# Kernel optimization log

Hardware: AMD Instinct MI355X
Metric: run time of the kernel (lower is better)

The kernel has to match this reference:

```python
import jax, jax.numpy as jnp
import numpy as np

B, M, F, U = 2048, 64, 512, 512  # batch, number_masks, num_features, units=ceil(F**1.0)

def setup_inputs() -> dict:
    key = jax.random.key(0)
    kx, kw = jax.random.split(key)
    x = jax.random.normal(kx, (B, M, F), dtype=jnp.float32)
    # glorot-uniform style init like keras Dense default
    limit = np.sqrt(6.0 / (F + U)).astype(np.float32)
    W = jax.random.uniform(kw, (M, F, U), dtype=jnp.float32, minval=-limit, maxval=limit)
    b = jnp.zeros((M, U), dtype=jnp.float32)
    return {"x": x, "W": W, "b": b}

def reference(x, W, b):
    # Per-mask Dense applied in a Python loop in the original == one batched GEMM.
    # y[b,m,u] = relu(sum_f x[b,m,f] * W[m,f,u] + b[m,u])
    y = jax.nn.relu(jnp.einsum('bmf,mfu->bmu', x, W) + b[None, :, :])
    # Concatenate along feature axis -> [B, M*U]
    return y.reshape(y.shape[0], -1)
```

## Files before the change

### kernel.cpp

```cpp
#include <hip/hip_runtime.h>
#include <hip/hip_bf16.h>


typedef __attribute__((ext_vector_type(8))) short bf16x8;
typedef __attribute__((ext_vector_type(4))) float f32x4;

#define LDS_S 40

__device__ __forceinline__ unsigned pk_bf16(float a, float b) {
    float2 t; t.x = a; t.y = b;
    __hip_bfloat162 h = __float22bfloat162_rn(t);
    union { __hip_bfloat162 h; unsigned u; } cv;
    cv.h = h;
    return cv.u;
}

__device__ __forceinline__ void gld16(const void* g, void* l) {
    __builtin_amdgcn_global_load_lds(
        (const __attribute__((address_space(1))) void*)g,
        (__attribute__((address_space(3))) void*)l, 16, 0, 0);
}

__global__ void wt_prep_kernel(const float* __restrict__ W, short* __restrict__ Wt) {
    __shared__ short t[64][80];
    const int m   = blockIdx.z;
    const int f0  = blockIdx.y * 64;
    const int u0  = blockIdx.x * 64;
    const int tid = threadIdx.x;
    const int fl  = tid >> 4;
    const int us  = tid & 15;
    #pragma unroll
    for (int i = 0; i < 4; ++i) {
        const int f = fl + 16 * i;
        float4 v = *(const float4*)(W + ((size_t)m * 512 + f0 + f) * 512 + u0 + us * 4);
        t[us * 4 + 0][f] = (short)(pk_bf16(v.x, v.x) & 0xffff);
        t[us * 4 + 1][f] = (short)(pk_bf16(v.y, v.y) & 0xffff);
        t[us * 4 + 2][f] = (short)(pk_bf16(v.z, v.z) & 0xffff);
        t[us * 4 + 3][f] = (short)(pk_bf16(v.w, v.w) & 0xffff);
    }
    __syncthreads();
    const int ur = tid >> 3;
    const int fs = tid & 7;
    #pragma unroll
    for (int i = 0; i < 2; ++i) {
        const int u = ur + 32 * i;
        *(uint4*)(Wt + ((size_t)m * 512 + u0 + u) * 512 + f0 + fs * 8) =
            *(const uint4*)&t[u][fs * 8];
    }
}

__global__ __launch_bounds__(256, 3) void pdense_main(const float* __restrict__ X,
                                                      const short* __restrict__ Wt,
                                                      const float* __restrict__ bias,
                                                      float* __restrict__ Out) {
    __shared__ float ldsA[2][128 * 32];
    __shared__ short ldsB[2][128 * 32];

    const int tid  = threadIdx.x;
    const int lane = tid & 63;
    const int wave = tid >> 6;
    const int q    = lane >> 4;
    const int ln   = lane & 15;
    const int wr   = (wave >> 1) * 64;
    const int wc   = (wave & 1) * 64;

    const int id   = blockIdx.x;
    const int xcd  = id & 7;
    const int slot = id >> 3;
    const int m    = xcd * 8 + (slot >> 6);
    const int rem  = slot & 63;
    const int bt   = rem >> 2;
    const int ut   = rem & 3;
    const int row0 = bt * 128;
    const int col0 = ut * 128;

    const int arow = wave * 32 + (lane >> 3);
    const int ac   = (lane & 7) ^ (lane >> 3);
    const float* agp = X + (size_t)(row0 + arow) * 32768 + m * 512 + ac * 4;
    const int brow = wave * 32 + (lane >> 2);
    const int bc   = (lane & 3) ^ ((lane >> 3) & 3);
    const short* bgp = Wt + (size_t)m * 262144 + (size_t)(col0 + brow) * 512 + bc * 8;

    f32x4 acc[4][4];
    #pragma unroll
    for (int i = 0; i < 4; ++i)
        #pragma unroll
        for (int j = 0; j < 4; ++j)
            acc[i][j] = (f32x4)0.0f;

    #pragma unroll
    for (int i = 0; i < 4; ++i)
        gld16(agp + (size_t)i * 8 * 32768, &ldsA[0][(wave * 32 + i * 8) * 32]);
    #pragma unroll
    for (int j = 0; j < 2; ++j)
        gld16(bgp + (size_t)j * 16 * 512, &ldsB[0][(wave * 32 + j * 16) * 32]);

    const int s1 = (ln >> 1) & 3;
    const int s0 = ln & 1;

    for (int kt = 0; kt < 16; ++kt) {
        const int p = kt & 1;

        __builtin_amdgcn_sched_barrier(0);
        __builtin_amdgcn_s_barrier();
        __builtin_amdgcn_sched_barrier(0);

        if (kt + 1 < 16) {
            const int ko = (kt + 1) * 32;
            #pragma unroll
            for (int i = 0; i < 4; ++i)
                gld16(agp + ko + (size_t)i * 8 * 32768, &ldsA[p ^ 1][(wave * 32 + i * 8) * 32]);
            #pragma unroll
            for (int j = 0; j < 2; ++j)
                gld16(bgp + ko + (size_t)j * 16 * 512, &ldsB[p ^ 1][(wave * 32 + j * 16) * 32]);
            __builtin_amdgcn_sched_barrier(0);
            asm volatile("s_waitcnt vmcnt(6)" ::: "memory");
        } else {
            asm volatile("s_waitcnt vmcnt(0)" ::: "memory");
        }
        __builtin_amdgcn_sched_barrier(0);

        __builtin_amdgcn_s_barrier();
        __builtin_amdgcn_sched_barrier(0);

        bf16x8 aF[4], bF[4];
        #pragma unroll
        for (int i = 0; i < 4; ++i) {
            const int r = wr + i * 16 + ln;
            const float* base = &ldsA[p][r * 32 + ((q ^ s1) << 3)];
            float4 ca = *(const float4*)(base + (s0 << 2));
            float4 cb = *(const float4*)(base + ((1 - s0) << 2));
            union { bf16x8 v; uint4 u; } fr;
            fr.u.x = pk_bf16(ca.x, ca.y);
            fr.u.y = pk_bf16(ca.z, ca.w);
            fr.u.z = pk_bf16(cb.x, cb.y);
            fr.u.w = pk_bf16(cb.z, cb.w);
            aF[i] = fr.v;
        }
        #pragma unroll
        for (int j = 0; j < 4; ++j) {
            const int r = wc + j * 16 + ln;
            bF[j] = *(const bf16x8*)&ldsB[p][r * 32 + ((q ^ s1) << 3)];
        }
        #pragma unroll
        for (int i = 0; i < 4; ++i)
            #pragma unroll
            for (int j = 0; j < 4; ++j)
                acc[i][j] = __builtin_amdgcn_mfma_f32_16x16x32_bf16(aF[i], bF[j], acc[i][j], 0, 0, 0);
    }

    #pragma unroll
    for (int j = 0; j < 4; ++j) {
        const int c = col0 + wc + j * 16 + ln;
        const float bv = bias[m * 512 + c];
        #pragma unroll
        for (int i = 0; i < 4; ++i) {
            const int r = row0 + wr + i * 16 + q * 4;
            float* op = Out + (size_t)r * 32768 + m * 512 + c;
            f32x4 v = acc[i][j];
            #pragma unroll
            for (int t = 0; t < 4; ++t) {
                float val = v[t] + bv;
                op[(size_t)t * 32768] = val > 0.0f ? val : 0.0f;
            }
        }
    }
}

__global__ void pdense_fallback(const float* __restrict__ X,
                                const float* __restrict__ Wp,
                                const float* __restrict__ bias,
                                float* __restrict__ Out) {
    __shared__ short ldsA[128 * LDS_S];
    __shared__ short ldsB[128 * LDS_S];

    const int tid  = threadIdx.x;
    const int lane = tid & 63;
    const int wave = tid >> 6;
    const int q    = lane >> 4;
    const int ln   = lane & 15;
    const int wr   = (wave >> 1) * 64;
    const int wc   = (wave & 1) * 64;

    const int m    = blockIdx.y;
    const int bt   = blockIdx.x & 15;
    const int ut   = blockIdx.x >> 4;
    const int row0 = bt * 128;
    const int col0 = ut * 128;

    const int ar0 = tid >> 2;
    const int ak0 = (tid & 3) * 8;
    const int ar1 = ar0 + 64;
    const float* aP0 = X + (size_t)(row0 + ar0) * 32768 + m * 512 + ak0;
    const float* aP1 = X + (size_t)(row0 + ar1) * 32768 + m * 512 + ak0;

    const int k0 = (tid & 7) * 4;
    const int u0 = (tid >> 3) * 4;
    const float* bP = Wp + (size_t)m * 262144 + (size_t)k0 * 512 + col0 + u0;

    f32x4 acc[4][4];
    #pragma unroll
    for (int i = 0; i < 4; ++i)
        #pragma unroll
        for (int j = 0; j < 4; ++j)
            acc[i][j] = (f32x4)0.0f;

    float4 a_pre[2][2];
    float4 b_pre[4];

    a_pre[0][0] = ((const float4*)aP0)[0];
    a_pre[0][1] = ((const float4*)aP0)[1];
    a_pre[1][0] = ((const float4*)aP1)[0];
    a_pre[1][1] = ((const float4*)aP1)[1];
    #pragma unroll
    for (int i = 0; i < 4; ++i)
        b_pre[i] = *(const float4*)(bP + (size_t)i * 512);

    for (int kt = 0; kt < 16; ++kt) {
        {
            uint4 w0, w1;
            w0.x = pk_bf16(a_pre[0][0].x, a_pre[0][0].y);
            w0.y = pk_bf16(a_pre[0][0].z, a_pre[0][0].w);
            w0.z = pk_bf16(a_pre[0][1].x, a_pre[0][1].y);
            w0.w = pk_bf16(a_pre[0][1].z, a_pre[0][1].w);
            *(uint4*)&ldsA[ar0 * LDS_S + ak0] = w0;
            w1.x = pk_bf16(a_pre[1][0].x, a_pre[1][0].y);
            w1.y = pk_bf16(a_pre[1][0].z, a_pre[1][0].w);
            w1.z = pk_bf16(a_pre[1][1].x, a_pre[1][1].y);
            w1.w = pk_bf16(a_pre[1][1].z, a_pre[1][1].w);
            *(uint4*)&ldsA[ar1 * LDS_S + ak0] = w1;
            #pragma unroll
            for (int j = 0; j < 4; ++j) {
                float c0 = ((const float*)&b_pre[0])[j];
                float c1 = ((const float*)&b_pre[1])[j];
                float c2 = ((const float*)&b_pre[2])[j];
                float c3 = ((const float*)&b_pre[3])[j];
                uint2 wv;
                wv.x = pk_bf16(c0, c1);
                wv.y = pk_bf16(c2, c3);
                *(uint2*)&ldsB[(u0 + j) * LDS_S + k0] = wv;
            }
        }
        __syncthreads();

        if (kt + 1 < 16) {
            const int ko = (kt + 1) * 32;
            a_pre[0][0] = ((const float4*)(aP0 + ko))[0];
            a_pre[0][1] = ((const float4*)(aP0 + ko))[1];
            a_pre[1][0] = ((const float4*)(aP1 + ko))[0];
            a_pre[1][1] = ((const float4*)(aP1 + ko))[1];
            #pragma unroll
            for (int i = 0; i < 4; ++i)
                b_pre[i] = *(const float4*)(bP + (size_t)(ko + i) * 512);
        }

        bf16x8 aF[4], bF[4];
        #pragma unroll
        for (int i = 0; i < 4; ++i)
            aF[i] = *(const bf16x8*)&ldsA[(wr + i * 16 + ln) * LDS_S + q * 8];
        #pragma unroll
        for (int j = 0; j < 4; ++j)
            bF[j] = *(const bf16x8*)&ldsB[(wc + j * 16 + ln) * LDS_S + q * 8];
        #pragma unroll
        for (int i = 0; i < 4; ++i)
            #pragma unroll
            for (int j = 0; j < 4; ++j)
                acc[i][j] = __builtin_amdgcn_mfma_f32_16x16x32_bf16(aF[i], bF[j], acc[i][j], 0, 0, 0);

        __syncthreads();
    }

    #pragma unroll
    for (int j = 0; j < 4; ++j) {
        const int c = col0 + wc + j * 16 + ln;
        const float bv = bias[m * 512 + c];
        #pragma unroll
        for (int i = 0; i < 4; ++i) {
            const int r = row0 + wr + i * 16 + q * 4;
            float* op = Out + (size_t)r * 32768 + m * 512 + c;
            f32x4 v = acc[i][j];
            #pragma unroll
            for (int t = 0; t < 4; ++t) {
                float val = v[t] + bv;
                op[(size_t)t * 32768] = val > 0.0f ? val : 0.0f;
            }
        }
    }
}

extern "C" void kernel_launch(void* const* d_in, const int* in_sizes, int n_in,
                              void* d_out, int out_size, void* d_ws, size_t ws_size,
                              hipStream_t stream) {
    const float* x    = (const float*)d_in[0];
    const float* W    = (const float*)d_in[1];
    const float* bias = (const float*)d_in[2];
    float* out = (float*)d_out;

    const size_t wt_bytes = (size_t)64 * 512 * 512 * sizeof(short);
    if (ws_size >= wt_bytes) {
        short* Wt = (short*)d_ws;
        hipLaunchKernelGGL(wt_prep_kernel, dim3(8, 8, 64), dim3(256), 0, stream, W, Wt);
        hipLaunchKernelGGL(pdense_main, dim3(4096), dim3(256), 0, stream, x, Wt, bias, out);
    } else {
        hipLaunchKernelGGL(pdense_fallback, dim3(64, 64), dim3(256), 0, stream, x, W, bias, out);
    }
}
```

Measured before the change: 575.7 us.

## Pre-convert X to bf16 per-mask layout and use triple-buffered bf16 GEMM kernel

Measured after the change: 626.4 us. 8.8% more time.

```diff
diff --git a/kernel.cpp b/kernel.cpp
--- a/kernel.cpp
+++ b/kernel.cpp
@@ -19,6 +19,24 @@
     __builtin_amdgcn_global_load_lds(
         (const __attribute__((address_space(1))) void*)g,
         (__attribute__((address_space(3))) void*)l, 16, 0, 0);
+}
+
+__global__ void x_prep_kernel(const float* __restrict__ X, short* __restrict__ Xp) {
+    const int m  = blockIdx.y;
+    const int b0 = blockIdx.x * 8;
+    const int t  = threadIdx.x;
+    const int r  = t >> 5;
+    const int c  = t & 31;
+    const float* src = X + ((size_t)(b0 + r) * 64 + m) * 512;
+    short* dst = Xp + (size_t)m * 1048576 + (size_t)(b0 + r) * 512;
+    #pragma unroll
+    for (int i = 0; i < 4; ++i) {
+        float4 v = *(const float4*)(src + (size_t)(c + i * 32) * 4);
+        uint2 w;
+        w.x = pk_bf16(v.x, v.y);
+        w.y = pk_bf16(v.z, v.w);
+        *(uint2*)(dst + (size_t)(c + i * 32) * 4) = w;
+    }
 }
 
 __global__ void wt_prep_kernel(const float* __restrict__ W, short* __restrict__ Wt) {
@@ -46,6 +64,119 @@
         const int u = ur + 32 * i;
         *(uint4*)(Wt + ((size_t)m * 512 + u0 + u) * 512 + f0 + fs * 8) =
             *(const uint4*)&t[u][fs * 8];
+    }
+}
+
+__global__ __launch_bounds__(256, 3) void pdense_main2(const short* __restrict__ Xp,
+                                                       const short* __restrict__ Wt,
+                                                       const float* __restrict__ bias,
+                                                       float* __restrict__ Out) {
+    __shared__ short lds[3][2][128 * 32];
+
+    const int tid  = threadIdx.x;
+    const int lane = tid & 63;
+    const int wave = tid >> 6;
+    const int q    = lane >> 4;
+    const int ln   = lane & 15;
+    const int wr   = (wave >> 1) * 64;
+    const int wc   = (wave & 1) * 64;
+
+    const int id   = blockIdx.x;
+    const int xcd  = id & 7;
+    const int slot = id >> 3;
+    const int m    = xcd * 8 + (slot >> 6);
+    const int rem  = slot & 63;
+    const int bt   = rem >> 2;
+    const int ut   = rem & 3;
+    const int row0 = bt * 128;
+    const int col0 = ut * 128;
+
+    const int srow = wave * 32 + (lane >> 2);
+    const int sc   = (lane & 3) ^ ((lane >> 3) & 3);
+    const short* agp = Xp + (size_t)m * 1048576 + (size_t)(row0 + srow) * 512 + sc * 8;
+    const short* bgp = Wt + (size_t)m * 262144 + (size_t)(col0 + srow) * 512 + sc * 8;
+
+    f32x4 acc[4][4];
+    #pragma unroll
+    for (int i = 0; i < 4; ++i)
+        #pragma unroll
+        for (int j = 0; j < 4; ++j)
+            acc[i][j] = (f32x4)0.0f;
+
+    #pragma unroll
+    for (int t = 0; t < 2; ++t) {
+        #pragma unroll
+        for (int j = 0; j < 2; ++j) {
+            gld16(agp + t * 32 + (size_t)j * 16 * 512, &lds[t][0][(wave * 32 + j * 16) * 32]);
+            gld16(bgp + t * 32 + (size_t)j * 16 * 512, &lds[t][1][(wave * 32 + j * 16) * 32]);
+        }
+    }
+
+    const int s1 = (ln >> 1) & 3;
+
+    #pragma unroll
+    for (int kt = 0; kt < 16; ++kt) {
+        const int cur = kt % 3;
+
+        __builtin_amdgcn_sched_barrier(0);
+        __builtin_amdgcn_s_barrier();
+        __builtin_amdgcn_sched_barrier(0);
+
+        if (kt + 2 < 16) {
+            const int nb = (kt + 2) % 3;
+            const int ko = (kt + 2) * 32;
+            #pragma unroll
+            for (int j = 0; j < 2; ++j) {
+                gld16(agp + ko + (size_t)j * 16 * 512, &lds[nb][0][(wave * 32 + j * 16) * 32]);
+                gld16(bgp + ko + (size_t)j * 16 * 512, &lds[nb][1][(wave * 32 + j * 16) * 32]);
+            }
+        }
+        __builtin_amdgcn_sched_barrier(0);
+        if (kt < 14) {
+            asm volatile("s_waitcnt vmcnt(8)" ::: "memory");
+        } else if (kt == 14) {
+            asm volatile("s_waitcnt vmcnt(4)" ::: "memory");
+        } else {
+            asm volatile("s_waitcnt vmcnt(0)" ::: "memory");
+        }
+        __builtin_amdgcn_sched_barrier(0);
+
+        __builtin_amdgcn_s_barrier();
+        __builtin_amdgcn_sched_barrier(0);
+
+        bf16x8 aF[4], bF[4];
+        #pragma unroll
+        for (int i = 0; i < 4; ++i) {
+            const int r = wr + i * 16 + ln;
+            aF[i] = *(const bf16x8*)&lds[cur][0][r * 32 + ((q ^ s1) << 3)];
+        }
+        #pragma unroll
+        for (int j = 0; j < 4; ++j) {
+            const int r = wc + j * 16 + ln;
+            bF[j] = *(const bf16x8*)&lds[cur][1][r * 32 + ((q ^ s1) << 3)];
+        }
+        #pragma unroll
+        for (int i = 0; i < 4; ++i)
+            #pragma unroll
+            for (int j = 0; j < 4; ++j)
+                acc[i][j] = __builtin_amdgcn_mfma_f32_16x16x32_bf16(aF[i], bF[j], acc[i][j], 0, 0, 0);
+    }
+
+    #pragma unroll
+    for (int j = 0; j < 4; ++j) {
+        const int c = col0 + wc + j * 16 + ln;
+        const float bv = bias[m * 512 + c];
+        #pragma unroll
+        for (int i = 0; i < 4; ++i) {
+            const int r = row0 + wr + i * 16 + q * 4;
+            float* op = Out + (size_t)r * 32768 + m * 512 + c;
+            f32x4 v = acc[i][j];
+            #pragma unroll
+            for (int t = 0; t < 4; ++t) {
+                float val = v[t] + bv;
+                op[(size_t)t * 32768] = val > 0.0f ? val : 0.0f;
+            }
+        }
     }
 }
 
@@ -297,7 +428,14 @@
     float* out = (float*)d_out;
 
     const size_t wt_bytes = (size_t)64 * 512 * 512 * sizeof(short);
-    if (ws_size >= wt_bytes) {
+    const size_t xp_bytes = (size_t)2048 * 64 * 512 * sizeof(short);
+    if (ws_size >= wt_bytes + xp_bytes) {
+        short* Wt = (short*)d_ws;
+        short* Xp = (short*)((char*)d_ws + wt_bytes);
+        hipLaunchKernelGGL(x_prep_kernel, dim3(256, 64), dim3(256), 0, stream, x, Xp);
+        hipLaunchKernelGGL(wt_prep_kernel, dim3(8, 8, 64), dim3(256), 0, stream, W, Wt);
+        hipLaunchKernelGGL(pdense_main2, dim3(4096), dim3(256), 0, stream, Xp, Wt, bias, out);
+    } else if (ws_size >= wt_bytes) {
         short* Wt = (short*)d_ws;
         hipLaunchKernelGGL(wt_prep_kernel, dim3(8, 8, 64), dim3(256), 0, stream, W, Wt);
         hipLaunchKernelGGL(pdense_main, dim3(4096), dim3(256), 0, stream, x, Wt, bias, out);
```

## Convert A to bf16 in registers before LDS and triple-buffer the K pipeline

Applied to the files above, without the earlier changes.

After: 581.6 us. About the same (+1.0%).

```diff
diff --git a/kernel.cpp b/kernel.cpp
--- a/kernel.cpp
+++ b/kernel.cpp
@@ -49,12 +49,11 @@
     }
 }
 
-__global__ __launch_bounds__(256, 3) void pdense_main(const float* __restrict__ X,
-                                                      const short* __restrict__ Wt,
-                                                      const float* __restrict__ bias,
-                                                      float* __restrict__ Out) {
-    __shared__ float ldsA[2][128 * 32];
-    __shared__ short ldsB[2][128 * 32];
+__global__ __launch_bounds__(256, 3) void pdense_main3(const float* __restrict__ X,
+                                                       const short* __restrict__ Wt,
+                                                       const float* __restrict__ bias,
+                                                       float* __restrict__ Out) {
+    __shared__ short lds[3][2][128 * 32];
 
     const int tid  = threadIdx.x;
     const int lane = tid & 63;
@@ -74,12 +73,20 @@
     const int row0 = bt * 128;
     const int col0 = ut * 128;
 
-    const int arow = wave * 32 + (lane >> 3);
-    const int ac   = (lane & 7) ^ (lane >> 3);
-    const float* agp = X + (size_t)(row0 + arow) * 32768 + m * 512 + ac * 4;
-    const int brow = wave * 32 + (lane >> 2);
-    const int bc   = (lane & 3) ^ ((lane >> 3) & 3);
-    const short* bgp = Wt + (size_t)m * 262144 + (size_t)(col0 + brow) * 512 + bc * 8;
+    const int ar  = wave * 32 + (lane >> 3);
+    const int ac4 = lane & 7;
+    const float* agp = X + (size_t)(row0 + ar) * 32768 + m * 512 + ac4 * 4;
+    int awoff[4];
+    #pragma unroll
+    for (int i = 0; i < 4; ++i) {
+        const int r   = ar + i * 8;
+        const int pos = (ac4 >> 1) ^ ((r >> 1) & 3);
+        awoff[i] = r * 32 + pos * 8 + (ac4 & 1) * 4;
+    }
+
+    const int srow = wave * 32 + (lane >> 2);
+    const int sc   = (lane & 3) ^ ((lane >> 3) & 3);
+    const short* bgp = Wt + (size_t)m * 262144 + (size_t)(col0 + srow) * 512 + sc * 8;
 
     f32x4 acc[4][4];
     #pragma unroll
@@ -88,38 +95,81 @@
         for (int j = 0; j < 4; ++j)
             acc[i][j] = (f32x4)0.0f;
 
-    #pragma unroll
-    for (int i = 0; i < 4; ++i)
-        gld16(agp + (size_t)i * 8 * 32768, &ldsA[0][(wave * 32 + i * 8) * 32]);
-    #pragma unroll
-    for (int j = 0; j < 2; ++j)
-        gld16(bgp + (size_t)j * 16 * 512, &ldsB[0][(wave * 32 + j * 16) * 32]);
+    float4 aA[4], aB[4];
+
+    auto aload = [&](int kt2, float4 (&d)[4]) {
+        const float* p = agp + kt2 * 32;
+        #pragma unroll
+        for (int i = 0; i < 4; ++i)
+            d[i] = *(const float4*)(p + (size_t)i * 8 * 32768);
+    };
+    auto astore = [&](int b, const float4 (&s)[4]) {
+        #pragma unroll
+        for (int i = 0; i < 4; ++i) {
+            uint2 w;
+            w.x = pk_bf16(s[i].x, s[i].y);
+            w.y = pk_bf16(s[i].z, s[i].w);
+            *(uint2*)&lds[b][0][awoff[i]] = w;
+        }
+    };
+    auto bload = [&](int kt2, int b) {
+        const short* p = bgp + kt2 * 32;
+        gld16(p,            &lds[b][1][(wave * 32) * 32]);
+        gld16(p + 16 * 512, &lds[b][1][(wave * 32 + 16) * 32]);
+    };
+
+    aload(0, aA);
+    __builtin_amdgcn_sched_barrier(0);
+    aload(1, aB);
+    __builtin_amdgcn_sched_barrier(0);
+    asm volatile("s_waitcnt vmcnt(4)" ::: "memory");
+    __builtin_amdgcn_sched_barrier(0);
+    astore(0, aA);
+    __builtin_amdgcn_sched_barrier(0);
+    aload(2, aA);
+    __builtin_amdgcn_sched_barrier(0);
+    asm volatile("s_waitcnt vmcnt(4)" ::: "memory");
+    __builtin_amdgcn_sched_barrier(0);
+    astore(1, aB);
+    __builtin_amdgcn_sched_barrier(0);
+    bload(0, 0);
+    bload(1, 1);
+    __builtin_amdgcn_sched_barrier(0);
 
     const int s1 = (ln >> 1) & 3;
-    const int s0 = ln & 1;
-
+
+    #pragma unroll
     for (int kt = 0; kt < 16; ++kt) {
-        const int p = kt & 1;
+        const int cur = kt % 3;
+        const int nb  = (kt + 2) % 3;
+        const bool evn = (kt & 1) == 0;
 
         __builtin_amdgcn_sched_barrier(0);
         __builtin_amdgcn_s_barrier();
         __builtin_amdgcn_sched_barrier(0);
 
-        if (kt + 1 < 16) {
-            const int ko = (kt + 1) * 32;
-            #pragma unroll
-            for (int i = 0; i < 4; ++i)
-                gld16(agp + ko + (size_t)i * 8 * 32768, &ldsA[p ^ 1][(wave * 32 + i * 8) * 32]);
-            #pragma unroll
-            for (int j = 0; j < 2; ++j)
-                gld16(bgp + ko + (size_t)j * 16 * 512, &ldsB[p ^ 1][(wave * 32 + j * 16) * 32]);
-            __builtin_amdgcn_sched_barrier(0);
-            asm volatile("s_waitcnt vmcnt(6)" ::: "memory");
+        if (kt < 15) {
+            asm volatile("s_waitcnt vmcnt(2)" ::: "memory");
         } else {
             asm volatile("s_waitcnt vmcnt(0)" ::: "memory");
         }
         __builtin_amdgcn_sched_barrier(0);
 
+        if (kt + 2 < 16) {
+            if (evn) astore(nb, aA); else astore(nb, aB);
+        }
+        __builtin_amdgcn_sched_barrier(0);
+        if (kt + 3 < 16) {
+            if (evn) aload(kt + 3, aB); else aload(kt + 3, aA);
+        }
+        __builtin_amdgcn_sched_barrier(0);
+        if (kt + 2 < 16) {
+            bload(kt + 2, nb);
+        }
+        __builtin_amdgcn_sched_barrier(0);
+        asm volatile("s_waitcnt lgkmcnt(0)" ::: "memory");
+        __builtin_amdgcn_sched_barrier(0);
+
         __builtin_amdgcn_s_barrier();
         __builtin_amdgcn_sched_barrier(0);
 
@@ -127,20 +177,12 @@
         #pragma unroll
         for (int i = 0; i < 4; ++i) {
             const int r = wr + i * 16 + ln;
-            const float* base = &ldsA[p][r * 32 + ((q ^ s1) << 3)];
-            float4 ca = *(const float4*)(base + (s0 << 2));
-            float4 cb = *(const float4*)(base + ((1 - s0) << 2));
-            union { bf16x8 v; uint4 u; } fr;
-            fr.u.x = pk_bf16(ca.x, ca.y);
-            fr.u.y = pk_bf16(ca.z, ca.w);
-            fr.u.z = pk_bf16(cb.x, cb.y);
-            fr.u.w = pk_bf16(cb.z, cb.w);
-            aF[i] = fr.v;
+            aF[i] = *(const bf16x8*)&lds[cur][0][r * 32 + ((q ^ s1) << 3)];
         }
         #pragma unroll
         for (int j = 0; j < 4; ++j) {
             const int r = wc + j * 16 + ln;
-            bF[j] = *(const bf16x8*)&ldsB[p][r * 32 + ((q ^ s1) << 3)];
+            bF[j] = *(const bf16x8*)&lds[cur][1][r * 32 + ((q ^ s1) << 3)];
         }
         #pragma unroll
         for (int i = 0; i < 4; ++i)
@@ -300,7 +342,7 @@
     if (ws_size >= wt_bytes) {
         short* Wt = (short*)d_ws;
         hipLaunchKernelGGL(wt_prep_kernel, dim3(8, 8, 64), dim3(256), 0, stream, W, Wt);
-        hipLaunchKernelGGL(pdense_main, dim3(4096), dim3(256), 0, stream, x, Wt, bias, out);
+        hipLaunchKernelGGL(pdense_main3, dim3(4096), dim3(256), 0, stream, x, Wt, bias, out);
     } else {
         hipLaunchKernelGGL(pdense_fallback, dim3(64, 64), dim3(256), 0, stream, x, W, bias, out);
     }
```
